# Optimization experiments

Hardware: AMD Instinct MI355X
Metric: run time of the kernel (lower is better)

## Reference

```python
import jax, jax.numpy as jnp
import numpy as np

N_EDGES = 16777216
NUM_SEG = 512
STRENGTH = 0.01
STD_WEIGHT = 0.5
EPS = 1e-6


def setup_inputs() -> dict:
    key = jax.random.key(0)
    k1, k2, k3, k4 = jax.random.split(key, 4)
    x = jax.random.normal(k1, (N_EDGES,), dtype=jnp.float32)
    idx = jax.random.randint(k2, (N_EDGES,), 0, NUM_SEG, dtype=jnp.int32)
    target_mean = jax.random.normal(k3, (NUM_SEG,), dtype=jnp.float32)
    target_std = jax.random.uniform(k4, (NUM_SEG,), dtype=jnp.float32)
    return {"x": x, "idx": idx, "target_mean": target_mean, "target_std": target_std}


def _segment_mean(v, idx, counts):
    s = jax.ops.segment_sum(v, idx, num_segments=NUM_SEG)
    return s / counts


def reference(x, idx, target_mean, target_std):
    # counts per edge type (guard against empty segments)
    counts = jax.ops.segment_sum(jnp.ones_like(x), idx, num_segments=NUM_SEG)
    counts = jnp.maximum(counts, 1.0)

    # segment mean of raw weights -> [NUM_SEG]
    mean_w = _segment_mean(x, idx, counts)

    # logspace std: two-pass mean/variance of log(|x| + eps) per segment
    log_x = jnp.log(jnp.abs(x) + EPS)
    mean_log = _segment_mean(log_x, idx, counts)            # [NUM_SEG]
    sq_diff = jnp.square(log_x - mean_log[idx])             # [N_EDGES]
    log_var = _segment_mean(sq_diff, idx, counts)           # [NUM_SEG]
    std_w = jnp.sqrt(log_var + EPS)

    mean_loss = jnp.mean(jnp.square(mean_w - target_mean))
    std_loss = jnp.mean(jnp.square(std_w - target_std))
    total = (1.0 - STD_WEIGHT) * mean_loss + STD_WEIGHT * std_loss
    return total * STRENGTH
```

## Files before the change

kernel.cpp:

```cpp
#include <hip/hip_runtime.h>
#include <hip/hip_bf16.h>

#define NSEG 512
#define EPSF 1e-6f
#define MAIN_GRID 2048
#define MAIN_BLOCK 256

#define SC_XL 256.0f
#define SC_L2 32.0f
#define BIAS_X 8.0f
#define BIAS_L 14.0f


__global__ __launch_bounds__(1024) void zero_ws_kernel(double* __restrict__ g) {
    int i = blockIdx.x * blockDim.x + threadIdx.x;
    if (i < 4 * NSEG) g[i] = 0.0;
}

__global__ __launch_bounds__(MAIN_BLOCK) void seg_stats_kernel(const float4* __restrict__ x4,
                                                               const int4* __restrict__ i4,
                                                               float* __restrict__ parts,
                                                               double* __restrict__ gacc,
                                                               int n4, int use_parts) {
    __shared__ unsigned long long hist[NSEG];

    for (int i = threadIdx.x; i < NSEG; i += MAIN_BLOCK) hist[i] = 0ull;
    __syncthreads();

    const int stride = gridDim.x * blockDim.x;
    for (int i = blockIdx.x * blockDim.x + threadIdx.x; i < n4; i += stride) {
        float4 xv = x4[i];
        int4 iv = i4[i];
#pragma unroll
        for (int c = 0; c < 4; ++c) {
            float v = (c == 0) ? xv.x : (c == 1) ? xv.y : (c == 2) ? xv.z : xv.w;
            int s   = (c == 0) ? iv.x : (c == 1) ? iv.y : (c == 2) ? iv.z : iv.w;
            float lx = __logf(fabsf(v) + EPSF);
            unsigned xq = (unsigned)(int)rintf(fmaf(v, SC_XL, BIAS_X * SC_XL));
            unsigned lq = (unsigned)(int)rintf(fmaf(lx, SC_XL, BIAS_L * SC_XL));
            unsigned l2q = (unsigned)(int)rintf(lx * lx * SC_L2);
            unsigned long long contrib = (1ull << 57) | ((unsigned long long)xq << 38) |
                                         ((unsigned long long)lq << 19) |
                                         (unsigned long long)l2q;
            atomicAdd(&hist[s], contrib);
        }
    }
    __syncthreads();

    for (int sg = threadIdx.x; sg < NSEG; sg += MAIN_BLOCK) {
        unsigned long long hv = hist[sg];
        double cnt = (double)(unsigned)(hv >> 57);
        double sx = (double)(unsigned)((hv >> 38) & 0x7FFFFull) * (1.0 / 256.0) - cnt * 8.0;
        double sl = (double)(unsigned)((hv >> 19) & 0x7FFFFull) * (1.0 / 256.0) - cnt * 14.0;
        double sl2 = (double)(unsigned)(hv & 0x7FFFFull) * (1.0 / 32.0);
        if (use_parts) {
            *(float4*)(parts + (size_t)blockIdx.x * (NSEG * 4) + (sg << 2)) =
                make_float4((float)cnt, (float)sx, (float)sl, (float)sl2);
        } else {
            if (cnt != 0.0) {
                unsafeAtomicAdd(&gacc[0 * NSEG + sg], cnt);
                unsafeAtomicAdd(&gacc[1 * NSEG + sg], sx);
                unsafeAtomicAdd(&gacc[2 * NSEG + sg], sl);
                unsafeAtomicAdd(&gacc[3 * NSEG + sg], sl2);
            }
        }
    }
}

#define RP_CHUNKS 32
__global__ __launch_bounds__(256) void reduce_partials_kernel(const float* __restrict__ parts,
                                                              double* __restrict__ gacc) {
    int eg = blockIdx.x & 7;
    int bc = blockIdx.x >> 3;
    int e = eg * 256 + threadIdx.x;
    int b0 = bc * (MAIN_GRID / RP_CHUNKS);
    double acc = 0.0;
    for (int b = 0; b < MAIN_GRID / RP_CHUNKS; ++b)
        acc += (double)parts[(size_t)(b0 + b) * (NSEG * 4) + e];
    unsafeAtomicAdd(&gacc[(e & 3) * NSEG + (e >> 2)], acc);
}

__global__ __launch_bounds__(512) void finalize_kernel(const double* __restrict__ gacc,
                                                       const float* __restrict__ tmean,
                                                       const float* __restrict__ tstd,
                                                       float* __restrict__ out) {
    int s = threadIdx.x;
    double cnt = gacc[s];
    double c = cnt > 1.0 ? cnt : 1.0;
    double mean_w = gacc[NSEG + s] / c;
    double mean_log = gacc[2 * NSEG + s] / c;
    double var = gacc[3 * NSEG + s] / c - mean_log * mean_log;
    if (var < 0.0) var = 0.0;
    double std_w = sqrt(var + 1e-6);
    double dm = mean_w - (double)tmean[s];
    double dsd = std_w - (double)tstd[s];
    double term = 0.5 * dm * dm + 0.5 * dsd * dsd;

#pragma unroll
    for (int off = 32; off > 0; off >>= 1) term += __shfl_down(term, off, 64);

    __shared__ double part[8];
    int wid = threadIdx.x >> 6;
    if ((threadIdx.x & 63) == 0) part[wid] = term;
    __syncthreads();
    if (threadIdx.x == 0) {
        double t = 0.0;
#pragma unroll
        for (int i = 0; i < 8; ++i) t += part[i];
        out[0] = (float)((t / (double)NSEG) * 0.01);
    }
}

extern "C" void kernel_launch(void* const* d_in, const int* in_sizes, int n_in,
                              void* d_out, int out_size, void* d_ws, size_t ws_size,
                              hipStream_t stream) {
    const float* x = (const float*)d_in[0];
    const int* idx = (const int*)d_in[1];
    const float* tmean = (const float*)d_in[2];
    const float* tstd = (const float*)d_in[3];
    float* out = (float*)d_out;

    double* gacc = (double*)d_ws;
    float* parts = (float*)((char*)d_ws + 4 * NSEG * sizeof(double));
    size_t need = 4 * NSEG * sizeof(double) + (size_t)MAIN_GRID * NSEG * 4 * sizeof(float);
    int use_parts = (ws_size >= need) ? 1 : 0;

    int n = in_sizes[0];
    int n4 = n / 4;

    zero_ws_kernel<<<2, 1024, 0, stream>>>(gacc);
    seg_stats_kernel<<<MAIN_GRID, MAIN_BLOCK, 0, stream>>>((const float4*)x, (const int4*)idx,
                                                           parts, gacc, n4, use_parts);
    if (use_parts)
        reduce_partials_kernel<<<8 * RP_CHUNKS, 256, 0, stream>>>(parts, gacc);
    finalize_kernel<<<1, 512, 0, stream>>>(gacc, tmean, tstd, out);
}
```

Baseline: 41.35 us.

## Split packed 64-bit LDS histogram into three 32-bit arrays and double-buffer loads into LDS

Replaces the single 64-bit packed shared-memory atomic per element with three 32-bit LDS atomics (count plus squared-log in one word, x and log in separate words). For the exact input size it adds a fast path that streams x and idx straight into LDS with global_load_lds and double buffering, overlapping global loads with the atomic histogram work. The cost is three times as many LDS atomic operations and a hand-managed waitcnt schedule that only runs when n4 equals grid times groups per block.

```diff
diff --git a/kernel.cpp b/kernel.cpp
--- a/kernel.cpp
+++ b/kernel.cpp
@@ -5,11 +5,14 @@
 #define EPSF 1e-6f
 #define MAIN_GRID 2048
 #define MAIN_BLOCK 256
+#define GROUPS_PER_BLOCK 2048
+#define FILLS 8
 
 #define SC_XL 256.0f
 #define SC_L2 32.0f
 #define BIAS_X 8.0f
 #define BIAS_L 14.0f
+#define M25 0x1FFFFFFu
 
 
 __global__ __launch_bounds__(1024) void zero_ws_kernel(double* __restrict__ g) {
@@ -17,42 +20,84 @@
     if (i < 4 * NSEG) g[i] = 0.0;
 }
 
+__device__ __forceinline__ void accum3(unsigned* __restrict__ hA, unsigned* __restrict__ hB,
+                                       unsigned* __restrict__ hC, float4 xv, int4 iv) {
+#pragma unroll
+    for (int c = 0; c < 4; ++c) {
+        float v = (c == 0) ? xv.x : (c == 1) ? xv.y : (c == 2) ? xv.z : xv.w;
+        int s   = (c == 0) ? iv.x : (c == 1) ? iv.y : (c == 2) ? iv.z : iv.w;
+        float lx = __logf(fabsf(v) + EPSF);
+        unsigned xq = (unsigned)(int)rintf(fmaf(v, SC_XL, BIAS_X * SC_XL));
+        unsigned lq = (unsigned)(int)rintf(fmaf(lx, SC_XL, BIAS_L * SC_XL));
+        unsigned l2q = (unsigned)(int)rintf(lx * lx * SC_L2);
+        atomicAdd(&hA[s], (1u << 25) | l2q);
+        atomicAdd(&hB[s], xq);
+        atomicAdd(&hC[s], lq);
+    }
+}
+
 __global__ __launch_bounds__(MAIN_BLOCK) void seg_stats_kernel(const float4* __restrict__ x4,
                                                                const int4* __restrict__ i4,
                                                                float* __restrict__ parts,
                                                                double* __restrict__ gacc,
-                                                               int n4, int use_parts) {
-    __shared__ unsigned long long hist[NSEG];
+                                                               int n4, int use_parts, int fast) {
+    __shared__ unsigned hA[NSEG], hB[NSEG], hC[NSEG];
+    __shared__ float4 xbuf[2][MAIN_BLOCK];
+    __shared__ int4 ibuf[2][MAIN_BLOCK];
 
-    for (int i = threadIdx.x; i < NSEG; i += MAIN_BLOCK) hist[i] = 0ull;
+    for (int i = threadIdx.x; i < NSEG; i += MAIN_BLOCK) {
+        hA[i] = 0u;
+        hB[i] = 0u;
+        hC[i] = 0u;
+    }
     __syncthreads();
 
-    const int stride = gridDim.x * blockDim.x;
-    for (int i = blockIdx.x * blockDim.x + threadIdx.x; i < n4; i += stride) {
-        float4 xv = x4[i];
-        int4 iv = i4[i];
+    if (fast) {
+        const int w = threadIdx.x >> 6;
+        const int lane = threadIdx.x & 63;
+        const int gbase = blockIdx.x * GROUPS_PER_BLOCK + w * 64 + lane;
+
+#define STAGE(f, buf)                                                                     \
+    {                                                                                     \
+        __builtin_amdgcn_global_load_lds(                                                 \
+            (const __attribute__((address_space(1))) void*)(x4 + gbase + (f) * MAIN_BLOCK), \
+            (__attribute__((address_space(3))) void*)&xbuf[buf][w * 64], 16, 0, 0);       \
+        __builtin_amdgcn_global_load_lds(                                                 \
+            (const __attribute__((address_space(1))) void*)(i4 + gbase + (f) * MAIN_BLOCK), \
+            (__attribute__((address_space(3))) void*)&ibuf[buf][w * 64], 16, 0, 0);       \
+    }
+
+        STAGE(0, 0);
+        STAGE(1, 1);
 #pragma unroll
-        for (int c = 0; c < 4; ++c) {
-            float v = (c == 0) ? xv.x : (c == 1) ? xv.y : (c == 2) ? xv.z : xv.w;
-            int s   = (c == 0) ? iv.x : (c == 1) ? iv.y : (c == 2) ? iv.z : iv.w;
-            float lx = __logf(fabsf(v) + EPSF);
-            unsigned xq = (unsigned)(int)rintf(fmaf(v, SC_XL, BIAS_X * SC_XL));
-            unsigned lq = (unsigned)(int)rintf(fmaf(lx, SC_XL, BIAS_L * SC_XL));
-            unsigned l2q = (unsigned)(int)rintf(lx * lx * SC_L2);
-            unsigned long long contrib = (1ull << 57) | ((unsigned long long)xq << 38) |
-                                         ((unsigned long long)lq << 19) |
-                                         (unsigned long long)l2q;
-            atomicAdd(&hist[s], contrib);
+        for (int f = 0; f < FILLS; ++f) {
+            if (f < FILLS - 1) {
+                asm volatile("s_waitcnt vmcnt(2)" ::: "memory");
+            } else {
+                asm volatile("s_waitcnt vmcnt(0)" ::: "memory");
+            }
+            __builtin_amdgcn_sched_barrier(0);
+            float4 xv = xbuf[f & 1][threadIdx.x];
+            int4 iv = ibuf[f & 1][threadIdx.x];
+            asm volatile("s_waitcnt lgkmcnt(0)" ::: "memory");
+            __builtin_amdgcn_sched_barrier(0);
+            if (f + 2 < FILLS) STAGE(f + 2, f & 1);
+            accum3(hA, hB, hC, xv, iv);
         }
+#undef STAGE
+    } else {
+        const int stride = gridDim.x * blockDim.x;
+        for (int i = blockIdx.x * blockDim.x + threadIdx.x; i < n4; i += stride)
+            accum3(hA, hB, hC, x4[i], i4[i]);
     }
     __syncthreads();
 
     for (int sg = threadIdx.x; sg < NSEG; sg += MAIN_BLOCK) {
-        unsigned long long hv = hist[sg];
-        double cnt = (double)(unsigned)(hv >> 57);
-        double sx = (double)(unsigned)((hv >> 38) & 0x7FFFFull) * (1.0 / 256.0) - cnt * 8.0;
-        double sl = (double)(unsigned)((hv >> 19) & 0x7FFFFull) * (1.0 / 256.0) - cnt * 14.0;
-        double sl2 = (double)(unsigned)(hv & 0x7FFFFull) * (1.0 / 32.0);
+        unsigned a = hA[sg];
+        double cnt = (double)(a >> 25);
+        double sl2 = (double)(a & M25) * (1.0 / 32.0);
+        double sx = (double)hB[sg] * (1.0 / 256.0) - cnt * 8.0;
+        double sl = (double)hC[sg] * (1.0 / 256.0) - cnt * 14.0;
         if (use_parts) {
             *(float4*)(parts + (size_t)blockIdx.x * (NSEG * 4) + (sg << 2)) =
                 make_float4((float)cnt, (float)sx, (float)sl, (float)sl2);
@@ -127,10 +172,11 @@
 
     int n = in_sizes[0];
     int n4 = n / 4;
+    int fast = (n4 == MAIN_GRID * GROUPS_PER_BLOCK) ? 1 : 0;
 
     zero_ws_kernel<<<2, 1024, 0, stream>>>(gacc);
     seg_stats_kernel<<<MAIN_GRID, MAIN_BLOCK, 0, stream>>>((const float4*)x, (const int4*)idx,
-                                                           parts, gacc, n4, use_parts);
+                                                           parts, gacc, n4, use_parts, fast);
     if (use_parts)
         reduce_partials_kernel<<<8 * RP_CHUNKS, 256, 0, stream>>>(parts, gacc);
     finalize_kernel<<<1, 512, 0, stream>>>(gacc, tmean, tstd, out);
```

New measurement: 43.60 us. 5.4% more time.
